# Performance work log

Hardware: AMD Instinct MI355X
Metric: run time of the kernel (lower is better)

The kernel has to match this reference:

```python
import jax, jax.numpy as jnp
import numpy as np
from jax import lax

D = 512
K = 5
HID = 2 * D
EPS = 1e-5


def layernorm(x, g, b):
    mu = jnp.mean(x, axis=-1, keepdims=True)
    var = jnp.mean((x - mu) ** 2, axis=-1, keepdims=True)
    return (x - mu) * lax.rsqrt(var + EPS) * g + b


def setup_inputs() -> dict:
    key = jax.random.key(0)
    ks = jax.random.split(key, 16)
    B, T = 8, 4096
    sc = lambda fan: 1.0 / np.sqrt(fan)
    return {
        "x": jax.random.normal(ks[0], (B, T, D), jnp.float32),
        "decay_logit": jnp.zeros((D,), jnp.float32),
        "W_out": jax.random.uniform(ks[1], (D, D), jnp.float32, -sc(D), sc(D)),
        "b_out": jax.random.uniform(ks[2], (D,), jnp.float32, -sc(D), sc(D)),
        "conv_w": jax.random.uniform(ks[3], (D, 1, K), jnp.float32, -sc(K), sc(K)),
        "conv_b": jax.random.uniform(ks[4], (D,), jnp.float32, -sc(K), sc(K)),
        "ln1_g": jnp.ones((D,), jnp.float32),
        "ln1_b": jnp.zeros((D,), jnp.float32),
        "ln2_g": jnp.ones((D,), jnp.float32),
        "ln2_b": jnp.zeros((D,), jnp.float32),
        "W1": jax.random.uniform(ks[5], (HID, D), jnp.float32, -sc(D), sc(D)),
        "b1": jax.random.uniform(ks[6], (HID,), jnp.float32, -sc(D), sc(D)),
        "W2": jax.random.uniform(ks[7], (D, HID), jnp.float32, -sc(HID), sc(HID)),
        "b2": jax.random.uniform(ks[8], (D,), jnp.float32, -sc(HID), sc(HID)),
    }


def retention_core(xn, decay_logit, W_out, b_out, conv_w, conv_b):
    # xn: [B, T, D]
    B, T, _ = xn.shape
    a = jax.nn.sigmoid(decay_logit)  # [D]

    def step(s, xt):  # s, xt: [B, D]
        s = a * s + (1.0 - a) * xt
        return s, s

    s0 = jnp.zeros((B, D), xn.dtype)
    _, ss = lax.scan(step, s0, jnp.swapaxes(xn, 0, 1))  # [T, B, D]
    ss = jnp.swapaxes(ss, 0, 1)  # [B, T, D]
    y_ret = jnp.einsum("btd,ed->bte", ss, W_out) + b_out

    # depthwise conv1d, 'same' padding (K odd)
    xc = jnp.swapaxes(xn, 1, 2)  # [B, D, T]
    pad = (K - 1) // 2
    y_loc = lax.conv_general_dilated(
        xc, conv_w, window_strides=(1,), padding=[(pad, pad)],
        feature_group_count=D, dimension_numbers=("NCH", "OIH", "NCH"))
    y_loc = jnp.swapaxes(y_loc + conv_b[None, :, None], 1, 2)  # [B, T, D]
    return y_ret + y_loc


def reference(x, decay_logit, W_out, b_out, conv_w, conv_b,
              ln1_g, ln1_b, ln2_g, ln2_b, W1, b1, W2, b2):
    y = retention_core(layernorm(x, ln1_g, ln1_b),
                       decay_logit, W_out, b_out, conv_w, conv_b)
    x = x + y
    h = layernorm(x, ln2_g, ln2_b)
    h = jax.nn.gelu(jnp.einsum("btd,hd->bth", h, W1) + b1, approximate=False)
    y = jnp.einsum("bth,dh->btd", h, W2) + b2
    return x + y
```

## Files before the change

### kernel.cpp

```cpp
#include <hip/hip_runtime.h>
#include <stdint.h>

typedef unsigned short u16;

#define DIM 512
#define HIDN 1024
#define TT 4096
#define BB 8
#define MM 32768
#define CH 128
#define CL 32

__device__ __forceinline__ u16 f2bf(float f) {
  union { float f; uint32_t u; } v; v.f = f;
  uint32_t u = v.u;
  uint32_t r = u + 0x7fffu + ((u >> 16) & 1u);
  return (u16)(r >> 16);
}
__device__ __forceinline__ float bf2f(u16 h) {
  union { uint32_t u; float f; } v; v.u = ((uint32_t)h) << 16; return v.f;
}

typedef __bf16 bf16x8 __attribute__((ext_vector_type(8)));
typedef float f32x4 __attribute__((ext_vector_type(4)));

__global__ __launch_bounds__(256) void prep_kernel(
    const float* __restrict__ wout, const float* __restrict__ w1,
    const float* __restrict__ w2, const float* __restrict__ dl,
    const float* __restrict__ convw,
    u16* __restrict__ wout_h, u16* __restrict__ w1_h, u16* __restrict__ w2_h,
    float* __restrict__ a, float* __restrict__ oma, float* __restrict__ aL,
    float* __restrict__ convwT) {
  int i = blockIdx.x * 256 + threadIdx.x;
  if (i < DIM * DIM) wout_h[i] = f2bf(wout[i]);
  if (i < HIDN * DIM) { w1_h[i] = f2bf(w1[i]); w2_h[i] = f2bf(w2[i]); }
  if (i < 5 * DIM) {
    int kk = i / DIM, n = i - kk * DIM;
    convwT[i] = convw[n * 5 + kk];
  }
  if (i < DIM) {
    float av = 1.0f / (1.0f + expf(-dl[i]));
    a[i] = av; oma[i] = 1.0f - av; aL[i] = powf(av, (float)CL);
  }
}

__global__ __launch_bounds__(256) void ln_rows(
    const float* __restrict__ xin, const float* __restrict__ g,
    const float* __restrict__ bvec, u16* __restrict__ out) {
  int lane = threadIdx.x & 63, wave = threadIdx.x >> 6;
  size_t row = (size_t)blockIdx.x * 4 + wave;
  const float4* xr = (const float4*)(xin + row * DIM);
  float4 v0 = xr[lane * 2 + 0];
  float4 v1 = xr[lane * 2 + 1];
  float s1 = v0.x + v0.y + v0.z + v0.w + v1.x + v1.y + v1.z + v1.w;
  float s2 = v0.x * v0.x + v0.y * v0.y + v0.z * v0.z + v0.w * v0.w
           + v1.x * v1.x + v1.y * v1.y + v1.z * v1.z + v1.w * v1.w;
#pragma unroll
  for (int o = 1; o < 64; o <<= 1) { s1 += __shfl_xor(s1, o); s2 += __shfl_xor(s2, o); }
  float mu = s1 * (1.0f / DIM);
  float var = s2 * (1.0f / DIM) - mu * mu;
  float rs = rsqrtf(var + 1e-5f);
  const float4* gr = (const float4*)g;
  const float4* br = (const float4*)bvec;
  float4 g0 = gr[lane * 2], g1 = gr[lane * 2 + 1];
  float4 b0 = br[lane * 2], b1 = br[lane * 2 + 1];
  uint32_t p0 = (uint32_t)f2bf((v0.x - mu) * rs * g0.x + b0.x) | ((uint32_t)f2bf((v0.y - mu) * rs * g0.y + b0.y) << 16);
  uint32_t p1 = (uint32_t)f2bf((v0.z - mu) * rs * g0.z + b0.z) | ((uint32_t)f2bf((v0.w - mu) * rs * g0.w + b0.w) << 16);
  uint32_t p2 = (uint32_t)f2bf((v1.x - mu) * rs * g1.x + b1.x) | ((uint32_t)f2bf((v1.y - mu) * rs * g1.y + b1.y) << 16);
  uint32_t p3 = (uint32_t)f2bf((v1.z - mu) * rs * g1.z + b1.z) | ((uint32_t)f2bf((v1.w - mu) * rs * g1.w + b1.w) << 16);
  uint4 pk; pk.x = p0; pk.y = p1; pk.z = p2; pk.w = p3;
  ((uint4*)(out + row * DIM))[lane] = pk;
}

__global__ __launch_bounds__(256) void scan_local(
    const u16* __restrict__ xn, const float* __restrict__ a,
    const float* __restrict__ oma, float* __restrict__ carry) {
  int idx = blockIdx.x * 256 + threadIdx.x;
  int dp = (idx & 255) * 2;
  int c = (idx >> 8) & (CH - 1);
  int b = idx >> 15;
  float a0 = a[dp], a1 = a[dp + 1], o0 = oma[dp], o1 = oma[dp + 1];
  const uint32_t* xp = (const uint32_t*)(xn + ((size_t)(b * TT + c * CL)) * DIM + dp);
  float s0 = 0.f, s1 = 0.f;
#pragma unroll
  for (int i = 0; i < CL; ++i) {
    uint32_t u = xp[(size_t)i * (DIM / 2)];
    s0 = fmaf(a0, s0, o0 * bf2f((u16)(u & 0xffffu)));
    s1 = fmaf(a1, s1, o1 * bf2f((u16)(u >> 16)));
  }
  float2 cv; cv.x = s0; cv.y = s1;
  *(float2*)&carry[((size_t)(b * CH + c)) * DIM + dp] = cv;
}

__global__ __launch_bounds__(256) void scan_carry(
    const float* __restrict__ carry, const float* __restrict__ aL,
    float* __restrict__ start) {
  int idx = blockIdx.x * 256 + threadIdx.x;
  int d = idx & (DIM - 1);
  int b = idx >> 9;
  float al = aL[d];
  float s = 0.f;
#pragma unroll 8
  for (int c = 0; c < CH; ++c) {
    size_t o = ((size_t)(b * CH + c)) * DIM + d;
    start[o] = s;
    s = fmaf(al, s, carry[o]);
  }
}

__global__ __launch_bounds__(256) void scan_emit(
    const u16* __restrict__ xn, const float* __restrict__ a,
    const float* __restrict__ oma, const float* __restrict__ start,
    u16* __restrict__ ss) {
  int idx = blockIdx.x * 256 + threadIdx.x;
  int dp = (idx & 255) * 2;
  int c = (idx >> 8) & (CH - 1);
  int b = idx >> 15;
  float a0 = a[dp], a1 = a[dp + 1], o0 = oma[dp], o1 = oma[dp + 1];
  const uint32_t* xp = (const uint32_t*)(xn + ((size_t)(b * TT + c * CL)) * DIM + dp);
  uint32_t* sp = (uint32_t*)(ss + ((size_t)(b * TT + c * CL)) * DIM + dp);
  float2 st = *(const float2*)&start[((size_t)(b * CH + c)) * DIM + dp];
  float s0 = st.x, s1 = st.y;
#pragma unroll
  for (int i = 0; i < CL; ++i) {
    uint32_t u = xp[(size_t)i * (DIM / 2)];
    s0 = fmaf(a0, s0, o0 * bf2f((u16)(u & 0xffffu)));
    s1 = fmaf(a1, s1, o1 * bf2f((u16)(u >> 16)));
    sp[(size_t)i * (DIM / 2)] = (uint32_t)f2bf(s0) | ((uint32_t)f2bf(s1) << 16);
  }
}

template <int Kd, int NCOL, int EPI>
__global__ __launch_bounds__(512, 2) void gemm_bt(
    const u16* __restrict__ A, const u16* __restrict__ Bmat,
    const float* __restrict__ bias, const float* __restrict__ resid,
    const u16* __restrict__ xn, const float* __restrict__ convwT,
    const float* __restrict__ convb, float* __restrict__ outf,
    u16* __restrict__ outh) {
  extern __shared__ __align__(16) u16 lds[];
  u16* sAb = lds;
  u16* sBb = lds + 32768;
  const int tid = threadIdx.x;
  const int lane = tid & 63, wave = tid >> 6;
  const int wm = wave >> 2;
  const int wn = wave & 3;
  const int rA = lane & 15, q = lane >> 4;
  const int lrow = lane >> 3;
  const int lslot = lane & 7;
  const int gk = ((lslot ^ lrow) & 7) * 8;

  const int lin = blockIdx.x;
  const int tile_col = (lin >> 3) & (NCOL - 1);
  const int tile_row = (lin & 7) + 8 * ((lin >> 3) / NCOL);
  const size_t rowTile = (size_t)tile_row * 256;
  const size_t colTile = (size_t)tile_col * 256;

  const u16* Abase = A + rowTile * Kd;
  const u16* Bbase = Bmat + colTile * Kd;

  f32x4 acc[8][4];
#pragma unroll
  for (int i = 0; i < 8; i++)
#pragma unroll
    for (int j = 0; j < 4; j++) acc[i][j] = (f32x4){0.f, 0.f, 0.f, 0.f};

  auto stage = [&](int kt, int buf) {
#pragma unroll
    for (int j = 0; j < 4; ++j) {
      const int g = j * 8 + wave;
      const u16* ga = Abase + (size_t)(g * 8 + lrow) * Kd + kt + gk;
      const u16* gb = Bbase + (size_t)(g * 8 + lrow) * Kd + kt + gk;
      __builtin_amdgcn_global_load_lds(
          (const __attribute__((address_space(1))) void*)ga,
          (__attribute__((address_space(3))) void*)(sAb + buf * 16384 + g * 512), 16, 0, 0);
      __builtin_amdgcn_global_load_lds(
          (const __attribute__((address_space(1))) void*)gb,
          (__attribute__((address_space(3))) void*)(sBb + buf * 16384 + g * 512), 16, 0, 0);
    }
  };

  constexpr int NT = Kd / 64;
  stage(0, 0);
  stage(64, 1);
  __asm__ __volatile__("s_waitcnt vmcnt(8)" ::: "memory");
  __asm__ __volatile__("s_barrier" ::: "memory");

  const int sw = rA & 7;
#pragma unroll 1
  for (int t = 0; t < NT; ++t) {
    const int p = t & 1;
    const u16* bufA = sAb + p * 16384 + (wm * 128 + rA) * 64;
    const u16* bufB = sBb + p * 16384 + (wn * 64 + rA) * 64;
    bf16x8 afr[8][2], bfr[4][2];

#pragma unroll
    for (int ni = 0; ni < 4; ++ni)
#pragma unroll
      for (int ks = 0; ks < 2; ++ks)
        bfr[ni][ks] = *(const bf16x8*)&bufB[ni * 1024 + (((ks * 4 + q) ^ sw) * 8)];
#pragma unroll
    for (int mi = 0; mi < 2; ++mi)
#pragma unroll
      for (int ks = 0; ks < 2; ++ks)
        afr[mi][ks] = *(const bf16x8*)&bufA[mi * 1024 + (((ks * 4 + q) ^ sw) * 8)];
    __asm__ __volatile__("s_barrier" ::: "memory");
    __asm__ __volatile__("s_waitcnt lgkmcnt(0)" ::: "memory");
    __builtin_amdgcn_s_setprio(1);
#pragma unroll
    for (int mi = 0; mi < 2; ++mi)
#pragma unroll
      for (int ni = 0; ni < 4; ++ni)
#pragma unroll
        for (int ks = 0; ks < 2; ++ks)
          acc[mi][ni] = __builtin_amdgcn_mfma_f32_16x16x32_bf16(bfr[ni][ks], afr[mi][ks], acc[mi][ni], 0, 0, 0);
    __builtin_amdgcn_s_setprio(0);
    __asm__ __volatile__("s_barrier" ::: "memory");

#pragma unroll
    for (int mi = 2; mi < 8; ++mi)
#pragma unroll
      for (int ks = 0; ks < 2; ++ks)
        afr[mi][ks] = *(const bf16x8*)&bufA[mi * 1024 + (((ks * 4 + q) ^ sw) * 8)];
    __asm__ __volatile__("s_barrier" ::: "memory");
    __asm__ __volatile__("s_waitcnt lgkmcnt(0)" ::: "memory");
    __builtin_amdgcn_s_setprio(1);
#pragma unroll
    for (int mi = 2; mi < 4; ++mi)
#pragma unroll
      for (int ni = 0; ni < 4; ++ni)
#pragma unroll
        for (int ks = 0; ks < 2; ++ks)
          acc[mi][ni] = __builtin_amdgcn_mfma_f32_16x16x32_bf16(bfr[ni][ks], afr[mi][ks], acc[mi][ni], 0, 0, 0);
    __builtin_amdgcn_s_setprio(0);
    __asm__ __volatile__("s_barrier" ::: "memory");

    if (t + 2 < NT) stage((t + 2) * 64, p);
    __builtin_amdgcn_s_setprio(1);
#pragma unroll
    for (int mi = 4; mi < 8; ++mi)
#pragma unroll
      for (int ni = 0; ni < 4; ++ni)
#pragma unroll
        for (int ks = 0; ks < 2; ++ks)
          acc[mi][ni] = __builtin_amdgcn_mfma_f32_16x16x32_bf16(bfr[ni][ks], afr[mi][ks], acc[mi][ni], 0, 0, 0);
    __builtin_amdgcn_s_setprio(0);
    if (t + 2 < NT) {
      __asm__ __volatile__("s_waitcnt vmcnt(8)" ::: "memory");
    } else if (t + 1 < NT) {
      __asm__ __volatile__("s_waitcnt vmcnt(0)" ::: "memory");
    }
    __asm__ __volatile__("s_barrier" ::: "memory");
  }

#pragma unroll
  for (int mi = 0; mi < 8; ++mi) {
    size_t m = rowTile + wm * 128 + mi * 16 + rA;
#pragma unroll
    for (int ni = 0; ni < 4; ++ni) {
      int n0 = (int)colTile + wn * 64 + ni * 16 + q * 4;
      f32x4 v = acc[mi][ni];
      float4 bv = *(const float4*)&bias[n0];
      float val0 = v[0] + bv.x, val1 = v[1] + bv.y, val2 = v[2] + bv.z, val3 = v[3] + bv.w;
      if constexpr (EPI == 0) {
        int tt = (int)(m & (TT - 1));
        float4 cb = *(const float4*)&convb[n0];
        float4 rv = *(const float4*)&resid[m * DIM + n0];
        val0 += cb.x + rv.x; val1 += cb.y + rv.y; val2 += cb.z + rv.z; val3 += cb.w + rv.w;
#pragma unroll
        for (int kk = 0; kk < 5; ++kk) {
          int ttc = tt + kk - 2;
          if (ttc >= 0 && ttc < TT) {
            uint2 xv = *(const uint2*)&xn[(m + (size_t)kk - 2) * DIM + n0];
            float4 wv = *(const float4*)&convwT[kk * DIM + n0];
            val0 = fmaf(wv.x, bf2f((u16)(xv.x & 0xffffu)), val0);
            val1 = fmaf(wv.y, bf2f((u16)(xv.x >> 16)), val1);
            val2 = fmaf(wv.z, bf2f((u16)(xv.y & 0xffffu)), val2);
            val3 = fmaf(wv.w, bf2f((u16)(xv.y >> 16)), val3);
          }
        }
        float4 ov; ov.x = val0; ov.y = val1; ov.z = val2; ov.w = val3;
        *(float4*)&outf[m * DIM + n0] = ov;
      } else if constexpr (EPI == 1) {
        const float isq2 = 0.70710678118654752f;
        float g0 = 0.5f * val0 * (1.0f + erff(val0 * isq2));
        float g1 = 0.5f * val1 * (1.0f + erff(val1 * isq2));
        float g2 = 0.5f * val2 * (1.0f + erff(val2 * isq2));
        float g3 = 0.5f * val3 * (1.0f + erff(val3 * isq2));
        uint2 pk;
        pk.x = (uint32_t)f2bf(g0) | ((uint32_t)f2bf(g1) << 16);
        pk.y = (uint32_t)f2bf(g2) | ((uint32_t)f2bf(g3) << 16);
        *(uint2*)&outh[m * HIDN + n0] = pk;
      } else {
        float4 rv = *(const float4*)&resid[m * DIM + n0];
        float4 ov;
        ov.x = val0 + rv.x; ov.y = val1 + rv.y; ov.z = val2 + rv.z; ov.w = val3 + rv.w;
        *(float4*)&outf[m * DIM + n0] = ov;
      }
    }
  }
}

extern "C" void kernel_launch(void* const* d_in, const int* in_sizes, int n_in,
                              void* d_out, int out_size, void* d_ws, size_t ws_size,
                              hipStream_t stream) {
  const float* x      = (const float*)d_in[0];
  const float* dl     = (const float*)d_in[1];
  const float* W_out  = (const float*)d_in[2];
  const float* b_out  = (const float*)d_in[3];
  const float* conv_w = (const float*)d_in[4];
  const float* conv_b = (const float*)d_in[5];
  const float* ln1_g  = (const float*)d_in[6];
  const float* ln1_b  = (const float*)d_in[7];
  const float* ln2_g  = (const float*)d_in[8];
  const float* ln2_b  = (const float*)d_in[9];
  const float* W1     = (const float*)d_in[10];
  const float* b1     = (const float*)d_in[11];
  const float* W2     = (const float*)d_in[12];
  const float* b2     = (const float*)d_in[13];

  char* ws = (char*)d_ws;
  u16*   wout_h = (u16*)(ws + 0);
  u16*   w1_h   = (u16*)(ws + 524288);
  u16*   w2_h   = (u16*)(ws + 1572864);
  float* a_buf  = (float*)(ws + 2621440);
  float* oma    = (float*)(ws + 2623488);
  float* aL     = (float*)(ws + 2625536);
  float* convwT = (float*)(ws + 2627584);
  float* carry  = (float*)(ws + (4u << 20));
  float* start  = (float*)(ws + 6291456);
  u16*   xn  = (u16*)(ws + (8u << 20));
  u16*   ssb = (u16*)(ws + (40u << 20));
  float* x1  = (float*)(ws + (72u << 20));
  u16*   h   = (u16*)(ws + (136u << 20));
  u16*   hg  = (u16*)(ws + (168u << 20));

  float* out = (float*)d_out;

  hipFuncSetAttribute(reinterpret_cast<const void*>(&gemm_bt<512, 2, 0>),
                      hipFuncAttributeMaxDynamicSharedMemorySize, 131072);
  hipFuncSetAttribute(reinterpret_cast<const void*>(&gemm_bt<512, 4, 1>),
                      hipFuncAttributeMaxDynamicSharedMemorySize, 131072);
  hipFuncSetAttribute(reinterpret_cast<const void*>(&gemm_bt<1024, 2, 2>),
                      hipFuncAttributeMaxDynamicSharedMemorySize, 131072);

  prep_kernel<<<2048, 256, 0, stream>>>(W_out, W1, W2, dl, conv_w, wout_h, w1_h, w2_h, a_buf, oma, aL, convwT);
  ln_rows<<<MM / 4, 256, 0, stream>>>(x, ln1_g, ln1_b, xn);
  scan_local<<<(BB * CH * DIM / 2) / 256, 256, 0, stream>>>(xn, a_buf, oma, carry);
  scan_carry<<<(BB * DIM) / 256, 256, 0, stream>>>(carry, aL, start);
  scan_emit<<<(BB * CH * DIM / 2) / 256, 256, 0, stream>>>(xn, a_buf, oma, start, ssb);
  gemm_bt<512, 2, 0><<<256, 512, 131072, stream>>>(ssb, wout_h, b_out, x, xn, convwT, conv_b, x1, nullptr);
  ln_rows<<<MM / 4, 256, 0, stream>>>(x1, ln2_g, ln2_b, h);
  gemm_bt<512, 4, 1><<<512, 512, 131072, stream>>>(h, w1_h, b1, nullptr, nullptr, nullptr, nullptr, nullptr, hg);
  gemm_bt<1024, 2, 2><<<256, 512, 131072, stream>>>(hg, w2_h, b2, x1, nullptr, nullptr, nullptr, out, nullptr);
}
```

Measured before the change: 401.8 us.

## Restructure GEMM main loop to single-stage prefetch with interleaved LDS reads

Replaces the two-tile-ahead global-to-LDS prefetch, with its several barriers per iteration, by a one-tile-ahead prefetch issued at the top of each iteration into the other buffer. A-fragment LDS reads for the next quarter are interleaved with the MFMAs of the current quarter. Each iteration now ends with one full vmcnt(0)/lgkmcnt(0) wait and a single barrier. This removes barrier overhead but shortens the lookahead for hiding global memory latency, and it relies on the compiler to order the LDS reads and the MFMAs.

```diff
diff --git a/kernel.cpp b/kernel.cpp
--- a/kernel.cpp
+++ b/kernel.cpp
@@ -181,8 +181,7 @@
 
   constexpr int NT = Kd / 64;
   stage(0, 0);
-  stage(64, 1);
-  __asm__ __volatile__("s_waitcnt vmcnt(8)" ::: "memory");
+  __asm__ __volatile__("s_waitcnt vmcnt(0)" ::: "memory");
   __asm__ __volatile__("s_barrier" ::: "memory");
 
   const int sw = rA & 7;
@@ -191,8 +190,10 @@
     const int p = t & 1;
     const u16* bufA = sAb + p * 16384 + (wm * 128 + rA) * 64;
     const u16* bufB = sBb + p * 16384 + (wn * 64 + rA) * 64;
-    bf16x8 afr[8][2], bfr[4][2];
-
+
+    if (t + 1 < NT) stage((t + 1) * 64, p ^ 1);
+
+    bf16x8 bfr[4][2], afr[8][2];
 #pragma unroll
     for (int ni = 0; ni < 4; ++ni)
 #pragma unroll
@@ -203,52 +204,28 @@
 #pragma unroll
       for (int ks = 0; ks < 2; ++ks)
         afr[mi][ks] = *(const bf16x8*)&bufA[mi * 1024 + (((ks * 4 + q) ^ sw) * 8)];
-    __asm__ __volatile__("s_barrier" ::: "memory");
-    __asm__ __volatile__("s_waitcnt lgkmcnt(0)" ::: "memory");
-    __builtin_amdgcn_s_setprio(1);
-#pragma unroll
-    for (int mi = 0; mi < 2; ++mi)
-#pragma unroll
-      for (int ni = 0; ni < 4; ++ni)
-#pragma unroll
-        for (int ks = 0; ks < 2; ++ks)
-          acc[mi][ni] = __builtin_amdgcn_mfma_f32_16x16x32_bf16(bfr[ni][ks], afr[mi][ks], acc[mi][ni], 0, 0, 0);
-    __builtin_amdgcn_s_setprio(0);
-    __asm__ __volatile__("s_barrier" ::: "memory");
-
-#pragma unroll
-    for (int mi = 2; mi < 8; ++mi)
-#pragma unroll
-      for (int ks = 0; ks < 2; ++ks)
-        afr[mi][ks] = *(const bf16x8*)&bufA[mi * 1024 + (((ks * 4 + q) ^ sw) * 8)];
-    __asm__ __volatile__("s_barrier" ::: "memory");
-    __asm__ __volatile__("s_waitcnt lgkmcnt(0)" ::: "memory");
-    __builtin_amdgcn_s_setprio(1);
-#pragma unroll
-    for (int mi = 2; mi < 4; ++mi)
-#pragma unroll
-      for (int ni = 0; ni < 4; ++ni)
-#pragma unroll
-        for (int ks = 0; ks < 2; ++ks)
-          acc[mi][ni] = __builtin_amdgcn_mfma_f32_16x16x32_bf16(bfr[ni][ks], afr[mi][ks], acc[mi][ni], 0, 0, 0);
-    __builtin_amdgcn_s_setprio(0);
-    __asm__ __volatile__("s_barrier" ::: "memory");
-
-    if (t + 2 < NT) stage((t + 2) * 64, p);
-    __builtin_amdgcn_s_setprio(1);
-#pragma unroll
-    for (int mi = 4; mi < 8; ++mi)
-#pragma unroll
-      for (int ni = 0; ni < 4; ++ni)
-#pragma unroll
-        for (int ks = 0; ks < 2; ++ks)
-          acc[mi][ni] = __builtin_amdgcn_mfma_f32_16x16x32_bf16(bfr[ni][ks], afr[mi][ks], acc[mi][ni], 0, 0, 0);
-    __builtin_amdgcn_s_setprio(0);
-    if (t + 2 < NT) {
-      __asm__ __volatile__("s_waitcnt vmcnt(8)" ::: "memory");
-    } else if (t + 1 < NT) {
-      __asm__ __volatile__("s_waitcnt vmcnt(0)" ::: "memory");
+
+#pragma unroll
+    for (int qd = 0; qd < 4; ++qd) {
+      if (qd < 3) {
+#pragma unroll
+        for (int mi = 2 * qd + 2; mi < 2 * qd + 4; ++mi)
+#pragma unroll
+          for (int ks = 0; ks < 2; ++ks)
+            afr[mi][ks] = *(const bf16x8*)&bufA[mi * 1024 + (((ks * 4 + q) ^ sw) * 8)];
+      }
+      __builtin_amdgcn_s_setprio(1);
+#pragma unroll
+      for (int mi = 2 * qd; mi < 2 * qd + 2; ++mi)
+#pragma unroll
+        for (int ni = 0; ni < 4; ++ni)
+#pragma unroll
+          for (int ks = 0; ks < 2; ++ks)
+            acc[mi][ni] = __builtin_amdgcn_mfma_f32_16x16x32_bf16(bfr[ni][ks], afr[mi][ks], acc[mi][ni], 0, 0, 0);
+      __builtin_amdgcn_s_setprio(0);
     }
+
+    __asm__ __volatile__("s_waitcnt lgkmcnt(0) vmcnt(0)" ::: "memory");
     __asm__ __volatile__("s_barrier" ::: "memory");
   }
 
```

Result: slower. 466.4 us (+16.1%).
